# Kernel tuning notes

Measured on AMD Instinct MI355X. Metric: run time of the kernel, lower is better.

## Reference

```python
import jax, jax.numpy as jnp
import numpy as np

NP = 8           # Np: prediction horizon
NUM_LAYERS = 2
HIDDEN = 1024    # hidden_dim
FEAT = 128       # input_dim == output_dim == nFeatures (closed-loop feedback)
NSAMPLES = 96
BATCH = 128


def setup_inputs() -> dict:
    key = jax.random.key(0)
    ks = jax.random.split(key, 13)
    s = 1.0 / np.sqrt(HIDDEN)
    u = lambda k, shape: jax.random.uniform(k, shape, jnp.float32, -s, s)
    return {
        "inMusic": jax.random.normal(ks[0], (NSAMPLES, BATCH, FEAT), jnp.float32),
        "h0": 0.1 * jax.random.normal(ks[1], (NUM_LAYERS, BATCH, HIDDEN), jnp.float32),
        "c0": 0.1 * jax.random.normal(ks[2], (NUM_LAYERS, BATCH, HIDDEN), jnp.float32),
        "W_ih_l0": u(ks[3], (4 * HIDDEN, FEAT)),
        "W_hh_l0": u(ks[4], (4 * HIDDEN, HIDDEN)),
        "b_ih_l0": u(ks[5], (4 * HIDDEN,)),
        "b_hh_l0": u(ks[6], (4 * HIDDEN,)),
        "W_ih_l1": u(ks[7], (4 * HIDDEN, HIDDEN)),
        "W_hh_l1": u(ks[8], (4 * HIDDEN, HIDDEN)),
        "b_ih_l1": u(ks[9], (4 * HIDDEN,)),
        "b_hh_l1": u(ks[10], (4 * HIDDEN,)),
        "W_lin": u(ks[11], (FEAT, HIDDEN)),
        "b_lin": u(ks[12], (FEAT,)),
    }


def _cell(x, h, c, Wih, Whh, bih, bhh):
    # PyTorch LSTM cell, gate order i, f, g, o
    g = x @ Wih.T + bih + h @ Whh.T + bhh                 # [B, 4H]
    i, f, gg, o = jnp.split(g, 4, axis=-1)
    c2 = jax.nn.sigmoid(f) * c + jax.nn.sigmoid(i) * jnp.tanh(gg)
    h2 = jax.nn.sigmoid(o) * jnp.tanh(c2)
    return h2, c2


def _forward(inMusic, h0, c0, W_ih_l0, W_hh_l0, b_ih_l0, b_hh_l0,
             W_ih_l1, W_hh_l1, b_ih_l1, b_hh_l1, W_lin, b_lin):
    nS, B, F = inMusic.shape
    layers = ((W_ih_l0, W_hh_l0, b_ih_l0, b_hh_l0),
              (W_ih_l1, W_hh_l1, b_ih_l1, b_hh_l1))

    @jax.checkpoint
    def stack_step(x, h, c):
        hs, cs, inp = [], [], x
        for li, (Wih, Whh, bih, bhh) in enumerate(layers):
            h2, c2 = _cell(inp, h[li], c[li], Wih, Whh, bih, bhh)
            hs.append(h2); cs.append(c2); inp = h2
        return jnp.stack(hs), jnp.stack(cs), inp

    linear = lambda x: x @ W_lin.T + b_lin

    def outer(carry, xs):
        hF, cF = carry
        xk, k = xs
        # filtering step (inner n == 0); runs only when min(k, Np) >= 1, i.e. k >= 1
        h1, c1, top = stack_step(xk, hF, cF)
        upd = k >= 1
        hF2 = jnp.where(upd, h1, hF)
        cF2 = jnp.where(upd, c1, cF)
        pred0 = linear(top)

        # closed-loop prediction steps n = 1..Np-1 (each reads the previous
        # step's linear output, which is what outMusic[k+n,:,:,n-1] holds)
        def inner(pc, _):
            hp, cp, pred = pc
            h2, c2, t2 = stack_step(pred, hp, cp)
            p2 = linear(t2)
            return (h2, c2, p2), p2

        _, preds_rest = jax.lax.scan(inner, (h1, c1, pred0), None, length=NP - 1)
        preds_k = jnp.concatenate([pred0[None], preds_rest], axis=0)   # [Np, B, F]
        return (hF2, cF2), (preds_k, pred0)

    (hF, cF), (preds, pred0s) = jax.lax.scan(outer, (h0, c0), (inMusic, jnp.arange(nS)))

    # triangular init: outMusic[k, :, :, n] = inMusic[k] for k < Np, n >= k
    tri = jnp.arange(NP)[:, None] <= jnp.arange(NP)[None, :]           # [k, n]
    fill = jnp.where(tri[:, None, None, :], inMusic[:NP, :, :, None], 0.0)
    outMusic = jnp.zeros((nS, B, F, NP), inMusic.dtype).at[:NP].set(fill)

    # scatter: outMusic[k+n+1, :, :, n] = preds[k, n] iff n < min(k, Np) and k+n+1 < nS
    kk = jnp.arange(nS)[:, None]
    nn = jnp.arange(NP)[None, :]
    rows = kk + nn + 1
    valid = (nn < jnp.minimum(kk, NP)) & (rows < nS)
    rows = jnp.where(valid, rows, nS).reshape(-1)                      # OOB -> dropped
    cols = jnp.broadcast_to(nn, (nS, NP)).reshape(-1)
    outMusic = outMusic.at[rows, :, :, cols].set(preds.reshape(nS * NP, B, F), mode="drop")

    nextSampleEst = pred0s[-1][None]                                   # [1, B, F]
    return outMusic, hF, cF, nextSampleEst


def reference(inMusic, h0, c0, W_ih_l0, W_hh_l0, b_ih_l0, b_hh_l0,
              W_ih_l1, W_hh_l1, b_ih_l1, b_hh_l1, W_lin, b_lin):
    return _forward(inMusic, h0, c0, W_ih_l0, W_hh_l0, b_ih_l0, b_hh_l0,
                    W_ih_l1, W_hh_l1, b_ih_l1, b_hh_l1, W_lin, b_lin)
```

## Files before the change

kernel.cpp:

```cpp
#include <hip/hip_runtime.h>

#define HID 1024
#define FEAT 128
#define BAT 128
#define NSAMP 96
#define NPRED 8
#define GD 4096
#define SLOTE ((size_t)BAT * HID)
#define PREDT 16384
#define CHUNK 8192

typedef unsigned short u16;
typedef unsigned int u32;
typedef unsigned long long u64;
typedef short bf16x8 __attribute__((ext_vector_type(8)));
typedef float f32x4 __attribute__((ext_vector_type(4)));

__device__ inline u16 f2bf(float f) {
    unsigned u = __float_as_uint(f);
    u += 0x7FFFu + ((u >> 16) & 1u);
    return (u16)(u >> 16);
}
__device__ inline float bf2f(u16 h) { return __uint_as_float(((unsigned)h) << 16); }
__device__ inline float fsig(float x) { return 1.0f / (1.0f + __expf(-x)); }
__device__ inline float ftanh(float x) { return 1.0f - 2.0f / (__expf(2.0f * x) + 1.0f); }

__device__ inline size_t fmoff(int row, int kk) {
    return (size_t)(kk >> 6) * CHUNK + (size_t)(row >> 6) * 4096
         + (size_t)((row >> 4) & 3) * 1024 + (size_t)((kk >> 5) & 1) * 512
         + (size_t)((kk >> 3) & 3) * 128 + (size_t)(row & 15) * 8 + (kk & 7);
}

__device__ inline void gl2lds16(const u16* g, u16* l) {
    __builtin_amdgcn_global_load_lds(
        (const __attribute__((address_space(1))) u32*)g,
        (__attribute__((address_space(3))) u32*)l, 16, 0, 0);
}

__device__ inline void cstore8(u16* p, u64 v) {
    __hip_atomic_store((__attribute__((address_space(1))) u64*)p, v,
                       __ATOMIC_RELAXED, __HIP_MEMORY_SCOPE_AGENT);
}

__device__ inline u64 pack4bf(u16 a, u16 b, u16 c, u16 d) {
    return (u64)a | ((u64)b << 16) | ((u64)c << 32) | ((u64)d << 48);
}

#define FLAGN (2 * 97 * 32 * 32)
__device__ inline void pollflag(const int* base) {
    const int tid = threadIdx.x;
    if (tid < 64) {
        long t = 0;
        for (;;) {
            int v = (tid < 32)
                ? __hip_atomic_load(base + tid * 32, __ATOMIC_RELAXED, __HIP_MEMORY_SCOPE_AGENT)
                : 1;
            if (__all(v != 0)) break;
            __builtin_amdgcn_s_sleep(1);
            if (++t > 3000000L) break;
        }
    }
    __builtin_amdgcn_s_barrier();
    __builtin_amdgcn_sched_barrier(0);
}

__device__ inline size_t pgoff(int q, int cp, int lane) {
    return (size_t)(q >> 1) * CHUNK
         + (size_t)(((cp >> 2) * 8) + ((cp & 3) * 2) + (q & 1)) * 512 + lane * 8;
}

union SMemA {
    u16 st[4][2][4096];
    float g[32][132];
};

__global__ __launch_bounds__(256, 1) void lstm_chain(
    const u16* __restrict__ inb,
    const u16* __restrict__ Wih0p, const u16* __restrict__ Whh0p,
    const u16* __restrict__ Wih1p, const u16* __restrict__ Whh1p,
    const float* __restrict__ bp0, const float* __restrict__ bp1,
    const float* __restrict__ c0,
    u16* __restrict__ chainH, u16* __restrict__ chainCb,
    float* __restrict__ h_std, float* __restrict__ c_std,
    int* __restrict__ flags)
{
    __shared__ SMemA sm;
    const int blk = blockIdx.x;
    const int l = blk >> 5, tn = blk & 31;
    const int tid = threadIdx.x;
    const int wave = tid >> 6, lane = tid & 63;
    const int wm = wave >> 1, wn = wave & 1;
    const int quad = lane >> 4, lc = lane & 15;
    const int rl = tid >> 3, ub = (tid & 7) * 4;

    const u16* BihS = (l ? Wih1p : Wih0p) + (size_t)tn * 128 * (l ? HID : FEAT);
    const u16* BhhS = (l ? Whh1p : Whh0p) + (size_t)tn * 128 * HID;
    const float* bias = l ? bp1 : bp0;
    auto fw = [&](int ll, int s) { return flags + ((size_t)(ll * 97 + s) * 32) * 32; };

    float creg[4][4];
#pragma unroll
    for (int i = 0; i < 4; ++i) {
        int lrow = (rl >> 4) * 64 + i * 16 + (rl & 15);
        float4 c4 = *(const float4*)(c0 + (size_t)l * SLOTE + (size_t)lrow * HID + tn * 32 + ub);
        creg[i][0] = c4.x; creg[i][1] = c4.y; creg[i][2] = c4.z; creg[i][3] = c4.w;
    }
    float bv[4];
#pragma unroll
    for (int j = 0; j < 4; ++j) bv[j] = bias[tn * 128 + wn * 64 + j * 16 + lc];

    const int frA = wm * 2048 + (quad * 16 + lc) * 8;
    const int frB = wn * 2048 + (quad * 16 + lc) * 8;

    for (int k = 0; k < NSAMP; ++k) {
        const int rk = (k <= 1) ? 0 : k;

        const u16 *A0, *B0, *A1s, *B1s; int KP0, NP; const int* gate;
        if (l == 0) {
            A0 = inb + (size_t)k * PREDT;              B0 = BihS; KP0 = 4;
            A1s = chainH + (size_t)rk * SLOTE;         B1s = BhhS; NP = 36;
            gate = fw(0, rk);
        } else {
            pollflag(fw(1, rk));
            A0 = chainH + (size_t)(97 + rk) * SLOTE;   B0 = BhhS; KP0 = 32;
            A1s = chainH + (size_t)(k + 1) * SLOTE;    B1s = BihS; NP = 64;
            gate = fw(0, k + 1);
        }
        const int qgate = KP0 - 3;

        auto issue = [&](int q, int buf) {
            const u16 *Ab, *Bb; int qq;
            if (q < KP0) { Ab = A0;  Bb = B0;  qq = q; }
            else         { Ab = A1s; Bb = B1s; qq = q - KP0; }
#pragma unroll
            for (int c2 = 0; c2 < 2; ++c2) {
                int cp = wave * 2 + c2;
                size_t go = pgoff(qq, cp, lane);
                gl2lds16(Ab + go, &sm.st[buf][0][cp * 512]);
                gl2lds16(Bb + go, &sm.st[buf][1][cp * 512]);
            }
        };

        issue(0, 0); issue(1, 1); issue(2, 2);

        f32x4 acc[4][4];
#pragma unroll
        for (int j = 0; j < 4; ++j) {
            f32x4 bvv = {bv[j], bv[j], bv[j], bv[j]};
#pragma unroll
            for (int i = 0; i < 4; ++i) acc[i][j] = bvv;
        }

        for (int q = 0; q < NP; ++q) {
            if (q + 2 < NP)      asm volatile("s_waitcnt vmcnt(8)" ::: "memory");
            else if (q + 1 < NP) asm volatile("s_waitcnt vmcnt(4)" ::: "memory");
            else                 asm volatile("s_waitcnt vmcnt(0)" ::: "memory");
            __builtin_amdgcn_s_barrier();
            __builtin_amdgcn_sched_barrier(0);
            if (q == qgate) pollflag(gate);
            if (q + 3 < NP) issue(q + 3, (q + 3) & 3);
            const u16* la = sm.st[q & 3][0];
            const u16* lb = sm.st[q & 3][1];
            bf16x8 aF[4], bF[4];
#pragma unroll
            for (int i = 0; i < 4; ++i)
                aF[i] = *(const bf16x8*)&la[frA + i * 512];
#pragma unroll
            for (int j = 0; j < 4; ++j)
                bF[j] = *(const bf16x8*)&lb[frB + j * 512];
#pragma unroll
            for (int i = 0; i < 4; ++i)
#pragma unroll
                for (int j = 0; j < 4; ++j)
                    acc[i][j] = __builtin_amdgcn_mfma_f32_16x16x32_bf16(aF[i], bF[j], acc[i][j], 0, 0, 0);
        }

        __syncthreads();
        size_t slotBase = (size_t)(l * 97 + k + 1) * SLOTE;
#pragma unroll 1
        for (int i = 0; i < 4; ++i) {
#pragma unroll
            for (int j = 0; j < 4; ++j)
#pragma unroll
                for (int r = 0; r < 4; ++r)
                    sm.g[wm * 16 + quad * 4 + r][wn * 64 + j * 16 + lc] = acc[i][j][r];
            asm volatile("s_waitcnt lgkmcnt(0)" ::: "memory");
            __builtin_amdgcn_s_barrier();
            __builtin_amdgcn_sched_barrier(0);
            int lrow = (rl >> 4) * 64 + i * 16 + (rl & 15);
            float c2v[4], h2v[4];
#pragma unroll
            for (int uu = 0; uu < 4; ++uu) {
                float4 gg = *(const float4*)&sm.g[rl][(ub + uu) * 4];
                float iv = fsig(gg.x), fv = fsig(gg.y), gv = ftanh(gg.z), ov = fsig(gg.w);
                float c2 = fv * creg[i][uu] + iv * gv;
                if (k != 0) creg[i][uu] = c2;
                c2v[uu] = c2;
                h2v[uu] = ov * ftanh(c2);
            }
            cstore8(chainH + slotBase + fmoff(lrow, tn * 32 + ub),
                    pack4bf(f2bf(h2v[0]), f2bf(h2v[1]), f2bf(h2v[2]), f2bf(h2v[3])));
            size_t pOff = slotBase + ((size_t)tn * 128 + lrow) * 32 + ub;
            *(ushort4*)(chainCb + pOff) =
                make_ushort4(f2bf(c2v[0]), f2bf(c2v[1]), f2bf(c2v[2]), f2bf(c2v[3]));
            if (k == 95) {
                size_t sOff = (size_t)l * SLOTE + (size_t)lrow * HID + tn * 32 + ub;
                *(float4*)(h_std + sOff) = make_float4(h2v[0], h2v[1], h2v[2], h2v[3]);
                *(float4*)(c_std + sOff) = make_float4(c2v[0], c2v[1], c2v[2], c2v[3]);
            }
            __builtin_amdgcn_s_barrier();
            __builtin_amdgcn_sched_barrier(0);
        }
        asm volatile("s_waitcnt vmcnt(0)" ::: "memory");
        __builtin_amdgcn_s_barrier();
        if (tid == 0)
            __hip_atomic_store((__attribute__((address_space(1))) int*)(fw(l, k + 1) + tn * 32),
                               1, __ATOMIC_RELAXED, __HIP_MEMORY_SCOPE_AGENT);
    }
}

struct GArgs {
    const u16* A1; const u16* A2;
    const u16 *B1, *B2;
    const float* bias;
    const u16* c_in; u16* cout_b;
    u16* h_out;
    u16* lin_out;
    int KP1, KP2;
    int as1, as2;
    int mode;
};

union SMemB {
    u16 st[3][2][4096];
    float g[32][132];
};

__global__ __launch_bounds__(256, 3) void gemm_lstm(GArgs g)
{
    __shared__ SMemB sm;
    const int tid = threadIdx.x;
    const int wave = tid >> 6, lane = tid & 63;
    const int wm = wave >> 1, wn = wave & 1;
    const int quad = lane >> 4, lc = lane & 15;
    const int tn = blockIdx.x & 31;
    const int tm0 = (blockIdx.x >> 5) * 4;
    const int frA = wm * 2048 + (quad * 16 + lc) * 8;
    const int frB = wn * 2048 + (quad * 16 + lc) * 8;

    const u16* B1p = g.B1 + (size_t)tn * g.KP1 * 4096;
    const u16* B2p = g.B2 + (size_t)tn * g.KP2 * 4096;
    const int NP = g.KP1 + g.KP2;

    for (int t = 0; t < 4; ++t) {
        const int tm = tm0 + t;
        const u16* A1t = g.A1 + (size_t)tm * g.as1;
        const u16* A2t = g.A2 + (size_t)tm * g.as2;

        auto issue = [&](int q, int buf) {
            const u16 *Ab, *Bb; int qq;
            if (q < g.KP1) { Ab = A1t; Bb = B1p; qq = q; }
            else           { Ab = A2t; Bb = B2p; qq = q - g.KP1; }
#pragma unroll
            for (int c2 = 0; c2 < 2; ++c2) {
                int cp = wave * 2 + c2;
                size_t go = pgoff(qq, cp, lane);
                gl2lds16(Ab + go, &sm.st[buf][0][cp * 512]);
                gl2lds16(Bb + go, &sm.st[buf][1][cp * 512]);
            }
        };

        f32x4 acc[4][4];
#pragma unroll
        for (int j = 0; j < 4; ++j) {
            float bvx = g.bias[tn * 128 + wn * 64 + j * 16 + lc];
            f32x4 bvv = {bvx, bvx, bvx, bvx};
#pragma unroll
            for (int i = 0; i < 4; ++i) acc[i][j] = bvv;
        }

        issue(0, 0);
        issue(1, 1);
        for (int q = 0; q < NP; ++q) {
            if (q + 1 < NP) asm volatile("s_waitcnt vmcnt(4)" ::: "memory");
            else            asm volatile("s_waitcnt vmcnt(0)" ::: "memory");
            __builtin_amdgcn_s_barrier();
            __builtin_amdgcn_sched_barrier(0);
            if (q + 2 < NP) issue(q + 2, (q + 2) % 3);
            const u16* la = sm.st[q % 3][0];
            const u16* lb = sm.st[q % 3][1];
            bf16x8 aF[4], bF[4];
#pragma unroll
            for (int i = 0; i < 4; ++i)
                aF[i] = *(const bf16x8*)&la[frA + i * 512];
#pragma unroll
            for (int j = 0; j < 4; ++j)
                bF[j] = *(const bf16x8*)&lb[frB + j * 512];
#pragma unroll
            for (int i = 0; i < 4; ++i)
#pragma unroll
                for (int j = 0; j < 4; ++j)
                    acc[i][j] = __builtin_amdgcn_mfma_f32_16x16x32_bf16(aF[i], bF[j], acc[i][j], 0, 0, 0);
        }
        __syncthreads();

        const int rl = tid >> 3, ub = (tid & 7) * 4;
#pragma unroll 1
        for (int i = 0; i < 4; ++i) {
#pragma unroll
            for (int j = 0; j < 4; ++j)
#pragma unroll
                for (int r = 0; r < 4; ++r)
                    sG_alias: ;
#pragma unroll
            for (int j = 0; j < 4; ++j)
#pragma unroll
                for (int r = 0; r < 4; ++r)
                    sm.g[wm * 16 + quad * 4 + r][wn * 64 + j * 16 + lc] = acc[i][j][r];
            __syncthreads();
            int lrow = (rl >> 4) * 64 + i * 16 + (rl & 15);
            size_t pOff = (size_t)tm * SLOTE + ((size_t)tn * 128 + lrow) * 32 + ub;
            ushort4 co = *(const ushort4*)(g.c_in + pOff);
            float cold[4] = {bf2f(co.x), bf2f(co.y), bf2f(co.z), bf2f(co.w)};
            float c2v[4], h2v[4];
#pragma unroll
            for (int uu = 0; uu < 4; ++uu) {
                float4 gg = *(const float4*)&sm.g[rl][(ub + uu) * 4];
                float iv = fsig(gg.x), fv = fsig(gg.y), gv = ftanh(gg.z), ov = fsig(gg.w);
                float c2 = fv * cold[uu] + iv * gv;
                c2v[uu] = c2;
                h2v[uu] = ov * ftanh(c2);
            }
            *(ushort4*)(g.cout_b + pOff) =
                make_ushort4(f2bf(c2v[0]), f2bf(c2v[1]), f2bf(c2v[2]), f2bf(c2v[3]));
            *(ushort4*)(g.h_out + (size_t)tm * SLOTE + fmoff(lrow, tn * 32 + ub)) =
                make_ushort4(f2bf(h2v[0]), f2bf(h2v[1]), f2bf(h2v[2]), f2bf(h2v[3]));
            __syncthreads();
        }
    }
}

__global__ __launch_bounds__(256, 3) void gemm_lin(GArgs g)
{
    __shared__ u16 st[3][2][4096];
    const int tid = threadIdx.x;
    const int wave = tid >> 6, lane = tid & 63;
    const int wm = wave >> 1, wn = wave & 1;
    const int quad = lane >> 4, lc = lane & 15;
    const int tm = blockIdx.x;
    const int frA = wm * 2048 + (quad * 16 + lc) * 8;
    const int frB = wn * 2048 + (quad * 16 + lc) * 8;

    const u16* A1t = g.A1 + (size_t)tm * g.as1;
    const int NP = g.KP1;

    auto issue = [&](int q, int buf) {
#pragma unroll
        for (int c2 = 0; c2 < 2; ++c2) {
            int cp = wave * 2 + c2;
            size_t go = pgoff(q, cp, lane);
            gl2lds16(A1t + go, &st[buf][0][cp * 512]);
            gl2lds16(g.B1 + go, &st[buf][1][cp * 512]);
        }
    };

    f32x4 acc[4][4];
#pragma unroll
    for (int j = 0; j < 4; ++j) {
        float bvx = g.bias[wn * 64 + j * 16 + lc];
        f32x4 bvv = {bvx, bvx, bvx, bvx};
#pragma unroll
        for (int i = 0; i < 4; ++i) acc[i][j] = bvv;
    }

    issue(0, 0);
    issue(1, 1);
    for (int q = 0; q < NP; ++q) {
        if (q + 1 < NP) asm volatile("s_waitcnt vmcnt(4)" ::: "memory");
        else            asm volatile("s_waitcnt vmcnt(0)" ::: "memory");
        __builtin_amdgcn_s_barrier();
        __builtin_amdgcn_sched_barrier(0);
        if (q + 2 < NP) issue(q + 2, (q + 2) % 3);
        const u16* la = st[q % 3][0];
        const u16* lb = st[q % 3][1];
        bf16x8 aF[4], bF[4];
#pragma unroll
        for (int i = 0; i < 4; ++i)
            aF[i] = *(const bf16x8*)&la[frA + i * 512];
#pragma unroll
        for (int j = 0; j < 4; ++j)
            bF[j] = *(const bf16x8*)&lb[frB + j * 512];
#pragma unroll
        for (int i = 0; i < 4; ++i)
#pragma unroll
            for (int j = 0; j < 4; ++j)
                acc[i][j] = __builtin_amdgcn_mfma_f32_16x16x32_bf16(aF[i], bF[j], acc[i][j], 0, 0, 0);
    }

#pragma unroll
    for (int i = 0; i < 4; ++i)
#pragma unroll
        for (int j = 0; j < 4; ++j)
#pragma unroll
            for (int r = 0; r < 4; ++r) {
                int grow = wm * 64 + i * 16 + quad * 4 + r;
                int gcol = wn * 64 + j * 16 + lc;
                g.lin_out[(size_t)tm * PREDT + fmoff(grow, gcol)] = f2bf(acc[i][j][r]);
            }
}

__global__ void convert_weight(const float* __restrict__ src, u16* __restrict__ dst,
                               int kshift, int permute, int total) {
    int idx = blockIdx.x * 256 + threadIdx.x;
    if (idx >= total) return;
    const int K = 1 << kshift;
    int kk = idx & (K - 1);
    int rr = (idx >> kshift) & 127;
    int s = idx >> (kshift + 7);
    int jp = s * 128 + rr;
    int srow = permute ? ((jp & 3) * HID + (jp >> 2)) : jp;
    dst[((size_t)s << (kshift + 7)) + fmoff(rr, kk)] =
        f2bf(src[((size_t)srow << kshift) + kk]);
}

__global__ void conv_input(const float* __restrict__ in, u16* __restrict__ inb) {
    int idx = blockIdx.x * 256 + threadIdx.x;
    int f = idx & 127;
    int b = (idx >> 7) & 127;
    int k = idx >> 14;
    inb[(size_t)k * PREDT + fmoff(b, f)] = f2bf(in[idx]);
}

__global__ void combine_bias(const float* __restrict__ bi, const float* __restrict__ bh,
                             float* __restrict__ dst) {
    int j = blockIdx.x * 256 + threadIdx.x;
    int s = (j & 3) * HID + (j >> 2);
    dst[j] = bi[s] + bh[s];
}

__global__ void init_state(const float* __restrict__ h0, u16* __restrict__ chainH) {
    int idx = blockIdx.x * 256 + threadIdx.x;
    int l = idx >> 17;
    int r = idx & (int)(SLOTE - 1);
    int b = r >> 10, hh = r & 1023;
    chainH[(size_t)l * 97 * SLOTE + fmoff(b, hh)] = f2bf(h0[idx]);
}

__global__ void init_flags(int* __restrict__ f) {
    int gid = blockIdx.x * 256 + threadIdx.x;
    if (gid >= FLAGN) return;
    int step = (gid >> 10) % 97;
    f[gid] = ((gid & 31) == 0 && step == 0) ? 1 : 0;
}

__global__ void copy_next(const u16* __restrict__ predsb, float* __restrict__ out) {
    int idx = blockIdx.x * 256 + threadIdx.x;
    int b = idx >> 7, f = idx & 127;
    out[idx] = bf2f(predsb[(size_t)95 * PREDT + fmoff(b, f)]);
}

__global__ void gather_out(const float* __restrict__ inMusic, const u16* __restrict__ predsb,
                           float* __restrict__ outM) {
    int idx = blockIdx.x * 256 + threadIdx.x;
    int n = idx & 7;
    int f = (idx >> 3) & 127;
    int b = (idx >> 10) & 127;
    int r = idx >> 17;
    float v = 0.0f;
    if (r < NPRED && n >= r) {
        v = inMusic[((size_t)r * BAT + b) * FEAT + f];
    } else {
        int k = r - n - 1;
        if (n < k)
            v = bf2f(predsb[((size_t)n * NSAMP + k) * PREDT + fmoff(b, f)]);
    }
    outM[idx] = v;
}

__global__ void zero_out(float* __restrict__ o, int nmax) {
    int idx = blockIdx.x * 256 + threadIdx.x;
    if (idx < nmax) o[idx] = 0.0f;
}

extern "C" void kernel_launch(void* const* d_in, const int* in_sizes, int n_in,
                              void* d_out, int out_size, void* d_ws, size_t ws_size,
                              hipStream_t stream) {
    (void)in_sizes; (void)n_in;
    const float* inMusic = (const float*)d_in[0];
    const float* h0   = (const float*)d_in[1];
    const float* c0   = (const float*)d_in[2];
    const float* Wih0 = (const float*)d_in[3];
    const float* Whh0 = (const float*)d_in[4];
    const float* bih0 = (const float*)d_in[5];
    const float* bhh0 = (const float*)d_in[6];
    const float* Wih1 = (const float*)d_in[7];
    const float* Whh1 = (const float*)d_in[8];
    const float* bih1 = (const float*)d_in[9];
    const float* bhh1 = (const float*)d_in[10];
    const float* Wlin = (const float*)d_in[11];
    const float* blin = (const float*)d_in[12];
    float* out = (float*)d_out;

    const size_t OUT_H = (size_t)NSAMP * BAT * FEAT * NPRED;
    const size_t OUT_C = OUT_H + 2 * SLOTE;
    const size_t OUT_NEXT = OUT_C + 2 * SLOTE;

    char* ws = (char*)d_ws;
    size_t off = 0;
    auto alloc = [&](size_t bytes) {
        void* p = ws + off;
        off = (off + bytes + 255) & ~(size_t)255;
        return p;
    };
    u16* Wih0p = (u16*)alloc((size_t)GD * FEAT * 2);
    u16* Whh0p = (u16*)alloc((size_t)GD * HID * 2);
    u16* Wih1p = (u16*)alloc((size_t)GD * HID * 2);
    u16* Whh1p = (u16*)alloc((size_t)GD * HID * 2);
    u16* Wlinb = (u16*)alloc((size_t)FEAT * HID * 2);
    float* bp0 = (float*)alloc(GD * 4);
    float* bp1 = (float*)alloc(GD * 4);
    u16* chainH  = (u16*)alloc((size_t)2 * 97 * SLOTE * 2);
    u16* chainCb = (u16*)alloc((size_t)2 * 97 * SLOTE * 2);
    u16* hp2 = (u16*)alloc((size_t)2 * (size_t)NSAMP * SLOTE * 2);
    u16* predsb = (u16*)alloc((size_t)NPRED * NSAMP * PREDT * 2);
    u16* inb = (u16*)alloc((size_t)NSAMP * PREDT * 2);
    int* flags = (int*)alloc((size_t)FLAGN * 4);

    if (off > ws_size) {
        zero_out<<<(out_size + 255) / 256, 256, 0, stream>>>(out, out_size);
        return;
    }

    convert_weight<<<(GD * FEAT + 255) / 256, 256, 0, stream>>>(Wih0, Wih0p, 7, 1, GD * FEAT);
    convert_weight<<<(GD * HID + 255) / 256, 256, 0, stream>>>(Whh0, Whh0p, 10, 1, GD * HID);
    convert_weight<<<(GD * HID + 255) / 256, 256, 0, stream>>>(Wih1, Wih1p, 10, 1, GD * HID);
    convert_weight<<<(GD * HID + 255) / 256, 256, 0, stream>>>(Whh1, Whh1p, 10, 1, GD * HID);
    convert_weight<<<(FEAT * HID + 255) / 256, 256, 0, stream>>>(Wlin, Wlinb, 10, 0, FEAT * HID);
    conv_input<<<(NSAMP * BAT * FEAT) / 256, 256, 0, stream>>>(inMusic, inb);
    combine_bias<<<GD / 256, 256, 0, stream>>>(bih0, bhh0, bp0);
    combine_bias<<<GD / 256, 256, 0, stream>>>(bih1, bhh1, bp1);
    init_state<<<(int)(2 * SLOTE) / 256, 256, 0, stream>>>(h0, chainH);
    init_flags<<<(FLAGN + 255) / 256, 256, 0, stream>>>(flags);

    lstm_chain<<<64, 256, 0, stream>>>(
        inb, Wih0p, Whh0p, Wih1p, Whh1p, bp0, bp1, c0,
        chainH, chainCb, out + OUT_H, out + OUT_C, flags);

    auto Hs = [&](int l, int s) { return chainH + ((size_t)l * 97 + s) * SLOTE; };
    auto Cs = [&](int l, int s) { return chainCb + ((size_t)l * 97 + s) * SLOTE; };

    u16* hbuf0[2] = {Hs(0, 1), Hs(1, 1)};
    u16* hbuf1[2] = {hp2, hp2 + (size_t)NSAMP * SLOTE};
    u16* cB[2] = {Cs(0, 1), Cs(1, 1)};

    auto mkLin = [&](const u16* src, u16* dst) {
        GArgs a = {};
        a.A1 = src; a.KP1 = 32; a.as1 = (int)SLOTE; a.KP2 = 0;
        a.B1 = Wlinb; a.bias = blin;
        a.lin_out = dst; a.mode = 1;
        return a;
    };
    auto mkB = [&](int l, const u16* A1, int kp1, int as1, const u16* A2, u16* nxt) {
        GArgs a = {};
        a.A1 = A1; a.KP1 = kp1; a.as1 = as1;
        a.A2 = A2; a.KP2 = 32; a.as2 = (int)SLOTE;
        a.B1 = (l == 0) ? Wih0p : Wih1p; a.B2 = (l == 0) ? Whh0p : Whh1p;
        a.bias = (l == 0) ? bp0 : bp1;
        a.c_in = cB[l]; a.cout_b = cB[l];
        a.h_out = nxt; a.mode = 0;
        return a;
    };

    gemm_lin<<<96, 256, 0, stream>>>(mkLin(hbuf0[1], predsb));
    copy_next<<<(BAT * FEAT) / 256, 256, 0, stream>>>(predsb, out + OUT_NEXT);

    for (int n = 1; n < NPRED; ++n) {
        u16* cur0 = (n & 1) ? hbuf0[0] : hbuf1[0];
        u16* cur1 = (n & 1) ? hbuf0[1] : hbuf1[1];
        u16* nxt0 = (n & 1) ? hbuf1[0] : hbuf0[0];
        u16* nxt1 = (n & 1) ? hbuf1[1] : hbuf0[1];
        const u16* pin = predsb + (size_t)(n - 1) * NSAMP * PREDT;
        u16* pout = predsb + (size_t)n * NSAMP * PREDT;
        gemm_lstm<<<768, 256, 0, stream>>>(mkB(0, pin, 4, PREDT, cur0, nxt0));
        gemm_lstm<<<768, 256, 0, stream>>>(mkB(1, nxt0, 32, (int)SLOTE, cur1, nxt1));
        gemm_lin<<<96, 256, 0, stream>>>(mkLin(nxt1, pout));
    }

    gather_out<<<(NSAMP * BAT * FEAT * NPRED) / 256, 256, 0, stream>>>(inMusic, predsb, out);
}
```

Baseline: 7.708 ms.

## Give each wave private LDS staging buffers and drop block barriers in LSTM chain

Each wave now loads its own A and B fragments into a private LDS region instead of sharing block-wide staging. This removes the per-k-step s_barrier, and flag polling becomes per-wave with no block barrier. The loop is double-buffered in registers, so fragment reads for step q+1 are issued before the MFMAs of step q. The cost is duplicated global-to-LDS traffic, since waves sharing wm or wn rows now each load the same data, which roughly doubles load volume. It also adds more outstanding vmcnt entries per wave.

```diff
diff --git a/kernel.cpp b/kernel.cpp
--- a/kernel.cpp
+++ b/kernel.cpp
@@ -47,21 +47,17 @@
 }
 
 #define FLAGN (2 * 97 * 32 * 32)
-__device__ inline void pollflag(const int* base) {
-    const int tid = threadIdx.x;
-    if (tid < 64) {
-        long t = 0;
-        for (;;) {
-            int v = (tid < 32)
-                ? __hip_atomic_load(base + tid * 32, __ATOMIC_RELAXED, __HIP_MEMORY_SCOPE_AGENT)
-                : 1;
-            if (__all(v != 0)) break;
-            __builtin_amdgcn_s_sleep(1);
-            if (++t > 3000000L) break;
-        }
-    }
-    __builtin_amdgcn_s_barrier();
-    __builtin_amdgcn_sched_barrier(0);
+__device__ inline void pollw(const int* base) {
+    const int lane = threadIdx.x & 63;
+    long t = 0;
+    for (;;) {
+        int v = (lane < 32)
+            ? __hip_atomic_load(base + lane * 32, __ATOMIC_RELAXED, __HIP_MEMORY_SCOPE_AGENT)
+            : 1;
+        if (__all(v != 0)) break;
+        __builtin_amdgcn_s_sleep(1);
+        if (++t > 3000000L) break;
+    }
 }
 
 __device__ inline size_t pgoff(int q, int cp, int lane) {
@@ -70,7 +66,7 @@
 }
 
 union SMemA {
-    u16 st[4][2][4096];
+    u16 st[4][4][2][2048];
     float g[32][132];
 };
 
@@ -109,9 +105,6 @@
 #pragma unroll
     for (int j = 0; j < 4; ++j) bv[j] = bias[tn * 128 + wn * 64 + j * 16 + lc];
 
-    const int frA = wm * 2048 + (quad * 16 + lc) * 8;
-    const int frB = wn * 2048 + (quad * 16 + lc) * 8;
-
     for (int k = 0; k < NSAMP; ++k) {
         const int rk = (k <= 1) ? 0 : k;
 
@@ -121,27 +114,29 @@
             A1s = chainH + (size_t)rk * SLOTE;         B1s = BhhS; NP = 36;
             gate = fw(0, rk);
         } else {
-            pollflag(fw(1, rk));
+            pollw(fw(1, rk));
             A0 = chainH + (size_t)(97 + rk) * SLOTE;   B0 = BhhS; KP0 = 32;
             A1s = chainH + (size_t)(k + 1) * SLOTE;    B1s = BihS; NP = 64;
             gate = fw(0, k + 1);
         }
-        const int qgate = KP0 - 3;
 
         auto issue = [&](int q, int buf) {
             const u16 *Ab, *Bb; int qq;
             if (q < KP0) { Ab = A0;  Bb = B0;  qq = q; }
             else         { Ab = A1s; Bb = B1s; qq = q - KP0; }
 #pragma unroll
-            for (int c2 = 0; c2 < 2; ++c2) {
-                int cp = wave * 2 + c2;
-                size_t go = pgoff(qq, cp, lane);
-                gl2lds16(Ab + go, &sm.st[buf][0][cp * 512]);
-                gl2lds16(Bb + go, &sm.st[buf][1][cp * 512]);
+            for (int i = 0; i < 4; ++i) {
+                gl2lds16(Ab + pgoff(qq, wm * 4 + i, lane), &sm.st[wave][buf][0][i * 512]);
+                gl2lds16(Bb + pgoff(qq, wn * 4 + i, lane), &sm.st[wave][buf][1][i * 512]);
             }
         };
-
-        issue(0, 0); issue(1, 1); issue(2, 2);
+        auto readf = [&](int buf, bf16x8 (&aF)[4], bf16x8 (&bF)[4]) {
+#pragma unroll
+            for (int i = 0; i < 4; ++i) {
+                aF[i] = *(const bf16x8*)&sm.st[wave][buf][0][i * 512 + lane * 8];
+                bF[i] = *(const bf16x8*)&sm.st[wave][buf][1][i * 512 + lane * 8];
+            }
+        };
 
         f32x4 acc[4][4];
 #pragma unroll
@@ -151,28 +146,33 @@
             for (int i = 0; i < 4; ++i) acc[i][j] = bvv;
         }
 
-        for (int q = 0; q < NP; ++q) {
-            if (q + 2 < NP)      asm volatile("s_waitcnt vmcnt(8)" ::: "memory");
-            else if (q + 1 < NP) asm volatile("s_waitcnt vmcnt(4)" ::: "memory");
-            else                 asm volatile("s_waitcnt vmcnt(0)" ::: "memory");
-            __builtin_amdgcn_s_barrier();
-            __builtin_amdgcn_sched_barrier(0);
-            if (q == qgate) pollflag(gate);
-            if (q + 3 < NP) issue(q + 3, (q + 3) & 3);
-            const u16* la = sm.st[q & 3][0];
-            const u16* lb = sm.st[q & 3][1];
-            bf16x8 aF[4], bF[4];
+        issue(0, 0); issue(1, 1); issue(2, 2);
+        bf16x8 aE[4], bE[4], aO[4], bO[4];
+        asm volatile("s_waitcnt vmcnt(16)" ::: "memory");
+        readf(0, aE, bE);
+
+        auto step = [&](int q, bf16x8 (&aC)[4], bf16x8 (&bC)[4],
+                               bf16x8 (&aN)[4], bf16x8 (&bN)[4]) {
+            const int nq = q + 3;
+            if (nq == KP0) pollw(gate);
+            if (nq < NP) issue(nq, nq & 3);
+            if (q + 1 < NP) {
+                const int lastI = (nq < NP) ? nq : (NP - 1);
+                const int infl = lastI - (q + 1);
+                if (infl >= 2)      asm volatile("s_waitcnt vmcnt(16)" ::: "memory");
+                else if (infl == 1) asm volatile("s_waitcnt vmcnt(8)"  ::: "memory");
+                else                asm volatile("s_waitcnt vmcnt(0)"  ::: "memory");
+                readf((q + 1) & 3, aN, bN);
+            }
 #pragma unroll
             for (int i = 0; i < 4; ++i)
-                aF[i] = *(const bf16x8*)&la[frA + i * 512];
-#pragma unroll
-            for (int j = 0; j < 4; ++j)
-                bF[j] = *(const bf16x8*)&lb[frB + j * 512];
-#pragma unroll
-            for (int i = 0; i < 4; ++i)
 #pragma unroll
                 for (int j = 0; j < 4; ++j)
-                    acc[i][j] = __builtin_amdgcn_mfma_f32_16x16x32_bf16(aF[i], bF[j], acc[i][j], 0, 0, 0);
+                    acc[i][j] = __builtin_amdgcn_mfma_f32_16x16x32_bf16(aC[i], bC[j], acc[i][j], 0, 0, 0);
+        };
+        for (int q = 0; q < NP; q += 2) {
+            step(q,     aE, bE, aO, bO);
+            step(q + 1, aO, bO, aE, bE);
         }
 
         __syncthreads();
@@ -307,11 +307,6 @@
         const int rl = tid >> 3, ub = (tid & 7) * 4;
 #pragma unroll 1
         for (int i = 0; i < 4; ++i) {
-#pragma unroll
-            for (int j = 0; j < 4; ++j)
-#pragma unroll
-                for (int r = 0; r < 4; ++r)
-                    sG_alias: ;
 #pragma unroll
             for (int j = 0; j < 4; ++j)
 #pragma unroll
```

Measured after the change: 9.598 ms. +24.5%, slower.
